# Kernel tuning notes

Hardware: AMD Instinct MI355X
Metric: run time of the kernel (lower is better)

The kernel has to match this reference:

```python
import jax, jax.numpy as jnp
import numpy as np

B, T, C = 2, 2048, 1024
NUM_HEADS, NUM_KV_HEADS, HEAD_DIM = 16, 8, 64
R = NUM_HEADS // NUM_KV_HEADS  # q heads per kv head
WINDOW = 512
HIDDEN = 4096
SOFT_CAP = 50.0


def setup_inputs() -> dict:
    key = jax.random.key(0)
    ks = jax.random.split(key, 10)
    std = 0.02
    return {
        "x": jax.random.normal(ks[0], (B, T, C), jnp.float32),
        "kurtosis_sum": jnp.zeros((), jnp.float32),
        "rms1_scale": jnp.zeros((C,), jnp.float32),
        "q_kernel": std * jax.random.normal(ks[1], (C, R, NUM_KV_HEADS, HEAD_DIM), jnp.float32),
        "k_kernel": std * jax.random.normal(ks[2], (C, NUM_KV_HEADS, HEAD_DIM), jnp.float32),
        "v_kernel": std * jax.random.normal(ks[3], (C, NUM_KV_HEADS, HEAD_DIM), jnp.float32),
        "out_kernel": std * jax.random.normal(ks[4], (R, NUM_KV_HEADS, HEAD_DIM, C), jnp.float32),
        "rms2_scale": jnp.zeros((C,), jnp.float32),
        "gate_kernel": std * jax.random.normal(ks[5], (C, HIDDEN), jnp.float32),
        "up_kernel": std * jax.random.normal(ks[6], (C, HIDDEN), jnp.float32),
        "down_kernel": std * jax.random.normal(ks[7], (HIDDEN, C), jnp.float32),
    }


def sine_table(features, length, max_timescale=1e6):
    fraction = jnp.arange(0, features, 2, dtype=jnp.float32) / features
    rot_freq = 1.0 / (max_timescale ** fraction)
    sinusoid = jnp.arange(length, dtype=jnp.float32)[:, None] * rot_freq[None, :]
    sinusoid = jnp.concatenate([sinusoid, sinusoid], axis=-1)  # (T, features)
    return jnp.sin(sinusoid), jnp.cos(sinusoid)


def rotate_half(x):
    x1, x2 = jnp.split(x, 2, axis=-1)
    return jnp.concatenate([-x2, x1], axis=-1)


def rms_norm(x, scale):
    var = jnp.mean(jnp.square(x.astype(jnp.float32)), axis=-1, keepdims=True)
    normed = (x * jax.lax.rsqrt(var + 1e-6)).astype(x.dtype)
    return normed * (1 + scale)


def excess_kurtosis(emb):
    mean = jnp.mean(emb, axis=-1, keepdims=True)
    std = jnp.std(emb, axis=-1, keepdims=True)
    centralized = emb - mean
    fourth = jnp.mean(centralized ** 4, axis=-1, keepdims=True)
    kurt = jnp.squeeze(fourth / (std ** 4 + 1e-6), axis=-1).reshape(-1) - 3
    return jnp.sum(jnp.maximum(kurt, 0.0))


def reference(x, kurtosis_sum, rms1_scale, q_kernel, k_kernel, v_kernel,
              out_kernel, rms2_scale, gate_kernel, up_kernel, down_kernel):
    Bc, Tc, Cc = x.shape
    # sliding-window causal mask: j <= i and |i - j| < WINDOW
    idx = jnp.arange(Tc)
    causal = idx[:, None] >= idx[None, :]
    band = jnp.abs(idx[:, None] - idx[None, :]) < WINDOW
    mask = (causal & band)[None, None, None]  # (1,1,1,T,T) for brhsd scores

    # --- attention ---
    attn_in = rms_norm(x, rms1_scale)
    q = jnp.einsum('bsm,mrhk->brhsk', attn_in, q_kernel)
    k = jnp.einsum('bdm,mhk->bhdk', attn_in, k_kernel)
    v = jnp.einsum('bdm,mhv->bhdv', attn_in, v_kernel)

    sin, cos = sine_table(HEAD_DIM, Tc, max_timescale=1e6)
    q = q * cos[None, None, None] + rotate_half(q) * sin[None, None, None]
    k = k * cos[None, None] + rotate_half(k) * sin[None, None]

    scale = jax.lax.rsqrt(jnp.asarray(HEAD_DIM, dtype=x.dtype))
    qk = jnp.einsum('brhsk,bhdk->brhsd', q, k) * scale
    qk = jnp.tanh(qk / SOFT_CAP) * SOFT_CAP
    probs = jax.nn.softmax(qk.astype(jnp.float32), where=mask).astype(x.dtype)
    qkv = jnp.einsum('brhsd,bhdv->brhsv', probs, v)
    attn_out = jnp.einsum('brhsv,rhvm->bsm', qkv, out_kernel)
    x = x + attn_out

    # --- SwiGLU MLP ---
    mlp_in = rms_norm(x, rms2_scale)
    gate = jax.nn.silu(mlp_in @ gate_kernel)
    up = mlp_in @ up_kernel
    x = x + (up * gate) @ down_kernel

    return (x, kurtosis_sum + excess_kurtosis(x))
```

## Files before the change

### kernel.cpp

```cpp
#include <hip/hip_runtime.h>
#include <hip/hip_bf16.h>

typedef __attribute__((ext_vector_type(8))) short short8;
typedef __attribute__((ext_vector_type(4))) float f32x4;
typedef __attribute__((ext_vector_type(4))) int int4v;
typedef __attribute__((ext_vector_type(8))) int int8v;

#define DEVFN static __device__ __forceinline__

DEVFN float bf2f(unsigned short u) {
    unsigned int i = ((unsigned int)u) << 16;
    float f; __builtin_memcpy(&f, &i, 4); return f;
}
DEVFN unsigned short f2bf(float f) {
    unsigned int i; __builtin_memcpy(&i, &f, 4);
    unsigned int r = i + 0x7fffu + ((i >> 16) & 1u);
    return (unsigned short)(r >> 16);
}
DEVFN unsigned char f2fp8(float f) {
    int r = __builtin_amdgcn_cvt_pk_fp8_f32(f, f, 0, false);
    return (unsigned char)(r & 0xff);
}
DEVFN float fastrcp(float x) { return __builtin_amdgcn_rcpf(x); }

DEVFN void load_lds16(const void* g, void* l) {
    __builtin_amdgcn_global_load_lds(
        (__attribute__((address_space(1))) void*)g,
        (__attribute__((address_space(3))) void*)l, 16, 0, 0);
}

DEVFN f32x4 mfma_fp8(int8v a, int8v b, f32x4 c) {
    return __builtin_amdgcn_mfma_scale_f32_16x16x128_f8f6f4(
        a, b, c, 0, 0, 0, 0x7F7F7F7F, 0, 0x7F7F7F7F);
}

constexpr int Bsz = 2, T = 2048, C = 1024;
constexpr int NH = 16, NKV = 8, HD = 64;
constexpr int HID = 4096;
constexpr int NTOK = Bsz * T;
constexpr size_t MiB = 1024 * 1024;

constexpr size_t OFF_WQKV = 0;
constexpr size_t OFF_WOUT = 4 * MiB;
constexpr size_t OFF_WGATE = 6 * MiB;
constexpr size_t OFF_WUP = 10 * MiB;
constexpr size_t OFF_WDOWN = 14 * MiB;
constexpr size_t OFF_XN1 = 18 * MiB;
constexpr size_t OFF_QKVP = 26 * MiB;
constexpr size_t OFF_P2 = 26 * MiB;
constexpr size_t OFF_QB = 58 * MiB;
constexpr size_t OFF_KB = 66 * MiB;
constexpr size_t OFF_VT = 70 * MiB;
constexpr size_t OFF_CTX = 74 * MiB;
constexpr size_t OFF_X2 = 82 * MiB;
constexpr size_t OFF_XN2 = 98 * MiB;
constexpr size_t OFF_G = 102 * MiB;
constexpr size_t OFF_P4 = 118 * MiB;

__global__ __launch_bounds__(256) void prep_kernel(
    const float* __restrict__ qk, const float* __restrict__ kk2,
    const float* __restrict__ vk, const float* __restrict__ ok,
    const float* __restrict__ gk, const float* __restrict__ uk,
    const float* __restrict__ dk,
    unsigned short* __restrict__ wqkv, unsigned short* __restrict__ wout,
    unsigned char* __restrict__ wgate, unsigned char* __restrict__ wup,
    unsigned char* __restrict__ wdown,
    const float* __restrict__ x, const float* __restrict__ rms1_scale,
    unsigned short* __restrict__ xn1) {
    __shared__ float t[32][33];
    __shared__ float red[4];
    int id = blockIdx.x;
    int tid = threadIdx.x;
    if (id >= 15360) {
        int row = id - 15360;
        const float4 v = *(const float4*)&x[(size_t)row * 1024 + tid * 4];
        float ss = v.x * v.x + v.y * v.y + v.z * v.z + v.w * v.w;
#pragma unroll
        for (int m = 32; m; m >>= 1) ss += __shfl_xor(ss, m, 64);
        if ((tid & 63) == 0) red[tid >> 6] = ss;
        __syncthreads();
        float tot = red[0] + red[1] + red[2] + red[3];
        float inv = rsqrtf(tot * (1.f / 1024.f) + 1e-6f);
        const float4 sc = *(const float4*)&rms1_scale[tid * 4];
        size_t o = (size_t)row * 1024 + tid * 4;
        xn1[o + 0] = f2bf(v.x * inv * (1.f + sc.x));
        xn1[o + 1] = f2bf(v.y * inv * (1.f + sc.y));
        xn1[o + 2] = f2bf(v.z * inv * (1.f + sc.z));
        xn1[o + 3] = f2bf(v.w * inv * (1.f + sc.w));
        return;
    }
    const float* in; int K, N, nx, base; int fp8 = 0;
    unsigned short* out16 = nullptr; unsigned char* out8 = nullptr;
    if (id < 1024)       { in = qk;  out16 = wqkv;                       K = 1024; N = 1024; nx = 32;  base = 0; }
    else if (id < 1536)  { in = kk2; out16 = wqkv + (size_t)1024 * 1024; K = 1024; N = 512;  nx = 16;  base = 1024; }
    else if (id < 2048)  { in = vk;  out16 = wqkv + (size_t)1536 * 1024; K = 1024; N = 512;  nx = 16;  base = 1536; }
    else if (id < 3072)  { in = ok;  out16 = wout;                       K = 1024; N = 1024; nx = 32;  base = 2048; }
    else if (id < 7168)  { in = gk;  out8 = wgate; fp8 = 1;              K = 1024; N = 4096; nx = 128; base = 3072; }
    else if (id < 11264) { in = uk;  out8 = wup; fp8 = 1;                K = 1024; N = 4096; nx = 128; base = 7168; }
    else                 { in = dk;  out8 = wdown; fp8 = 1;              K = 4096; N = 1024; nx = 32;  base = 11264; }
    int lid = id - base;
    int n0 = (lid % nx) * 32, k0 = (lid / nx) * 32;
    int tx = tid & 31, ty = tid >> 5;
#pragma unroll
    for (int i = 0; i < 4; i++)
        t[ty + 8 * i][tx] = in[(size_t)(k0 + ty + 8 * i) * N + n0 + tx];
    __syncthreads();
    if (fp8) {
#pragma unroll
        for (int i = 0; i < 4; i++)
            out8[(size_t)(n0 + ty + 8 * i) * K + k0 + tx] = f2fp8(t[tx][ty + 8 * i] * 16.f);
    } else {
#pragma unroll
        for (int i = 0; i < 4; i++)
            out16[(size_t)(n0 + ty + 8 * i) * K + k0 + tx] = f2bf(t[tx][ty + 8 * i]);
    }
}

__global__ __launch_bounds__(256) void gemm128(const unsigned short* __restrict__ A,
                                               const unsigned short* __restrict__ Bt,
                                               unsigned short* __restrict__ Cp,
                                               int N, int K, int lda, int ldb,
                                               size_t zA, size_t zB, size_t zC) {
    __shared__ __align__(16) unsigned short As[128 * 32];
    __shared__ __align__(16) unsigned short Bs[128 * 32];
    A += (size_t)blockIdx.z * zA;
    Bt += (size_t)blockIdx.z * zB;
    const int tid = threadIdx.x;
    const int lane = tid & 63, w = tid >> 6;
    const int quad = lane >> 4, l15 = lane & 15;
    const int wr = w >> 1, wc = w & 1;
    const int m0 = blockIdx.y * 128, n0 = blockIdx.x * 128;

    f32x4 acc[4][4];
#pragma unroll
    for (int i = 0; i < 4; i++)
#pragma unroll
        for (int j = 0; j < 4; j++) acc[i][j] = f32x4{0.f, 0.f, 0.f, 0.f};

    const int stRow = (w << 4) + (lane >> 2);
    const int stCol = (lane & 3) << 3;

    for (int kk = 0; kk < K; kk += 32) {
#pragma unroll
        for (int i = 0; i < 2; i++) {
            load_lds16(A + (size_t)(m0 + (i << 6) + stRow) * lda + kk + stCol,
                       &As[((i << 6) + (w << 4)) * 32]);
            load_lds16(Bt + (size_t)(n0 + (i << 6) + stRow) * ldb + kk + stCol,
                       &Bs[((i << 6) + (w << 4)) * 32]);
        }
        __syncthreads();
        short8 a[4], b[4];
#pragma unroll
        for (int mi = 0; mi < 4; mi++)
            a[mi] = *(const short8*)&As[(wr * 64 + mi * 16 + l15) * 32 + quad * 8];
#pragma unroll
        for (int ni = 0; ni < 4; ni++)
            b[ni] = *(const short8*)&Bs[(wc * 64 + ni * 16 + l15) * 32 + quad * 8];
#pragma unroll
        for (int mi = 0; mi < 4; mi++)
#pragma unroll
            for (int ni = 0; ni < 4; ni++)
                acc[mi][ni] = __builtin_amdgcn_mfma_f32_16x16x32_bf16(a[mi], b[ni], acc[mi][ni], 0, 0, 0);
        __syncthreads();
    }
#pragma unroll
    for (int mi = 0; mi < 4; mi++)
#pragma unroll
        for (int ni = 0; ni < 4; ni++)
#pragma unroll
            for (int r = 0; r < 4; r++) {
                int row = m0 + wr * 64 + mi * 16 + quad * 4 + r;
                int col = n0 + wc * 64 + ni * 16 + l15;
                Cp[(size_t)blockIdx.z * zC + (size_t)row * N + col] = f2bf(acc[mi][ni][r]);
            }
}

DEVFN int8v read_frag8(const unsigned char* buf, int rb, int quad) {
    int base = rb * 128;
    int h0 = (2 * quad) ^ (rb & 7);
    int h1 = (2 * quad + 1) ^ (rb & 7);
    int4v lo = *(const int4v*)&buf[base + h0 * 16];
    int4v hi = *(const int4v*)&buf[base + h1 * 16];
    return int8v{lo.x, lo.y, lo.z, lo.w, hi.x, hi.y, hi.z, hi.w};
}

__global__ __launch_bounds__(256) void gateup_kernel(const unsigned char* __restrict__ A,
                                                     const unsigned char* __restrict__ Bg,
                                                     const unsigned char* __restrict__ Bu,
                                                     unsigned char* __restrict__ out) {
    __shared__ __align__(16) unsigned char As[2][128 * 128];
    __shared__ __align__(16) unsigned char Gs[2][64 * 128];
    __shared__ __align__(16) unsigned char Us[2][64 * 128];
    const int tid = threadIdx.x;
    const int lane = tid & 63, w = tid >> 6;
    const int quad = lane >> 4, l15 = lane & 15;
    const int wr = w >> 1, wc = w & 1;
    const int m0 = blockIdx.y * 128, n0 = blockIdx.x * 64;

    f32x4 aG[4][2], aU[4][2];
#pragma unroll
    for (int i = 0; i < 4; i++)
#pragma unroll
        for (int j = 0; j < 2; j++) { aG[i][j] = f32x4{0.f, 0.f, 0.f, 0.f}; aU[i][j] = f32x4{0.f, 0.f, 0.f, 0.f}; }

    const int lrow = lane >> 3;
    const int hA = (lane & 7) ^ lrow;

    auto STAGE = [&](int t, int b) {
#pragma unroll
        for (int j = 0; j < 4; j++) {
            int i = w * 4 + j;
            int r = i * 8 + lrow;
            load_lds16(A + (size_t)(m0 + r) * 1024 + t * 128 + hA * 16, &As[b][i * 1024]);
        }
#pragma unroll
        for (int j = 0; j < 2; j++) {
            int i = w * 2 + j;
            int r = i * 8 + lrow;
            load_lds16(Bg + (size_t)(n0 + r) * 1024 + t * 128 + hA * 16, &Gs[b][i * 1024]);
            load_lds16(Bu + (size_t)(n0 + r) * 1024 + t * 128 + hA * 16, &Us[b][i * 1024]);
        }
    };

    STAGE(0, 0);
    STAGE(1, 1);

#pragma unroll
    for (int t = 0; t < 8; ++t) {
        if (t < 7) asm volatile("s_waitcnt vmcnt(8)\n\ts_barrier" ::: "memory");
        else       asm volatile("s_waitcnt vmcnt(0)\n\ts_barrier" ::: "memory");
        const int b = t & 1;
        int8v a[4], bg[2], bu[2];
#pragma unroll
        for (int mi = 0; mi < 4; mi++)
            a[mi] = read_frag8(As[b], wr * 64 + mi * 16 + l15, quad);
#pragma unroll
        for (int ni = 0; ni < 2; ni++) {
            bg[ni] = read_frag8(Gs[b], wc * 32 + ni * 16 + l15, quad);
            bu[ni] = read_frag8(Us[b], wc * 32 + ni * 16 + l15, quad);
        }
        asm volatile("s_waitcnt lgkmcnt(0)\n\ts_barrier" ::: "memory");
        if (t < 6) STAGE(t + 2, b);
        __builtin_amdgcn_sched_barrier(0);
        __builtin_amdgcn_s_setprio(1);
#pragma unroll
        for (int mi = 0; mi < 4; mi++)
#pragma unroll
            for (int ni = 0; ni < 2; ni++) {
                aG[mi][ni] = mfma_fp8(a[mi], bg[ni], aG[mi][ni]);
                aU[mi][ni] = mfma_fp8(a[mi], bu[ni], aU[mi][ni]);
            }
        __builtin_amdgcn_s_setprio(0);
    }
#pragma unroll
    for (int mi = 0; mi < 4; mi++)
#pragma unroll
        for (int ni = 0; ni < 2; ni++)
#pragma unroll
            for (int r = 0; r < 4; r++) {
                int row = m0 + wr * 64 + mi * 16 + quad * 4 + r;
                int col = n0 + wc * 32 + ni * 16 + l15;
                float vg = aG[mi][ni][r] * (1.f / 64.f);
                float vu = aU[mi][ni][r] * (1.f / 64.f);
                float s = vg * fastrcp(1.f + __expf(-vg));
                out[(size_t)row * 4096 + col] = f2fp8(s * vu * 8.f);
            }
}

__global__ __launch_bounds__(256) void down_gemm(const unsigned char* __restrict__ A,
                                                 const unsigned char* __restrict__ Bt,
                                                 unsigned short* __restrict__ Cp) {
    __shared__ __align__(16) unsigned char As[2][128 * 128];
    __shared__ __align__(16) unsigned char Bs[2][128 * 128];
    const int tid = threadIdx.x;
    const int lane = tid & 63, w = tid >> 6;
    const int quad = lane >> 4, l15 = lane & 15;
    const int wr = w >> 1, wc = w & 1;
    const int m0 = blockIdx.y * 128, n0 = blockIdx.x * 128;
    const int kbase = blockIdx.z * 2048;

    f32x4 acc[4][4];
#pragma unroll
    for (int i = 0; i < 4; i++)
#pragma unroll
        for (int j = 0; j < 4; j++) acc[i][j] = f32x4{0.f, 0.f, 0.f, 0.f};

    const int lrow = lane >> 3;
    const int hA = (lane & 7) ^ lrow;

    auto STAGE = [&](int t, int b) {
#pragma unroll
        for (int j = 0; j < 4; j++) {
            int i = w * 4 + j;
            int r = i * 8 + lrow;
            load_lds16(A + (size_t)(m0 + r) * 4096 + kbase + t * 128 + hA * 16, &As[b][i * 1024]);
            load_lds16(Bt + (size_t)(n0 + r) * 4096 + kbase + t * 128 + hA * 16, &Bs[b][i * 1024]);
        }
    };

    STAGE(0, 0);
    STAGE(1, 1);

#pragma unroll
    for (int t = 0; t < 16; ++t) {
        if (t < 15) asm volatile("s_waitcnt vmcnt(8)\n\ts_barrier" ::: "memory");
        else        asm volatile("s_waitcnt vmcnt(0)\n\ts_barrier" ::: "memory");
        const int b = t & 1;
        int8v a[4], bb[4];
#pragma unroll
        for (int mi = 0; mi < 4; mi++)
            a[mi] = read_frag8(As[b], wr * 64 + mi * 16 + l15, quad);
#pragma unroll
        for (int ni = 0; ni < 4; ni++)
            bb[ni] = read_frag8(Bs[b], wc * 64 + ni * 16 + l15, quad);
        asm volatile("s_waitcnt lgkmcnt(0)\n\ts_barrier" ::: "memory");
        if (t < 14) STAGE(t + 2, b);
        __builtin_amdgcn_sched_barrier(0);
        __builtin_amdgcn_s_setprio(1);
#pragma unroll
        for (int mi = 0; mi < 4; mi++)
#pragma unroll
            for (int ni = 0; ni < 4; ni++)
                acc[mi][ni] = mfma_fp8(a[mi], bb[ni], acc[mi][ni]);
        __builtin_amdgcn_s_setprio(0);
    }
    const size_t Z = (size_t)NTOK * 1024;
#pragma unroll
    for (int mi = 0; mi < 4; mi++)
#pragma unroll
        for (int ni = 0; ni < 4; ni++)
#pragma unroll
            for (int r = 0; r < 4; r++) {
                int row = m0 + wr * 64 + mi * 16 + quad * 4 + r;
                int col = n0 + wc * 64 + ni * 16 + l15;
                Cp[(size_t)blockIdx.z * Z + (size_t)row * 1024 + col] =
                    f2bf(acc[mi][ni][r] * (1.f / 128.f));
            }
}

__global__ __launch_bounds__(256) void reduce_out(const unsigned short* __restrict__ p,
                                                  const float* __restrict__ x,
                                                  const float* __restrict__ scale,
                                                  float* __restrict__ x2,
                                                  unsigned char* __restrict__ xn2,
                                                  const float* __restrict__ ksum,
                                                  float* __restrict__ outk) {
    __shared__ float red[4];
    int row = blockIdx.x, tid = threadIdx.x;
    if (row == 0 && tid == 0) outk[0] = ksum[0];
    size_t base = (size_t)row * 1024 + tid * 4;
    const size_t Z = (size_t)NTOK * 1024;
    float4 v = *(const float4*)&x[base];
#pragma unroll
    for (int z = 0; z < 2; z++) {
        ushort4 u = *(const ushort4*)&p[base + z * Z];
        v.x += bf2f(u.x); v.y += bf2f(u.y); v.z += bf2f(u.z); v.w += bf2f(u.w);
    }
    *(float4*)&x2[base] = v;
    float ss = v.x * v.x + v.y * v.y + v.z * v.z + v.w * v.w;
#pragma unroll
    for (int m = 32; m; m >>= 1) ss += __shfl_xor(ss, m, 64);
    if ((tid & 63) == 0) red[tid >> 6] = ss;
    __syncthreads();
    float tot = red[0] + red[1] + red[2] + red[3];
    float inv = rsqrtf(tot * (1.f / 1024.f) + 1e-6f) * 4.f;
    const float4 sc = *(const float4*)&scale[tid * 4];
    xn2[base + 0] = f2fp8(v.x * inv * (1.f + sc.x));
    xn2[base + 1] = f2fp8(v.y * inv * (1.f + sc.y));
    xn2[base + 2] = f2fp8(v.z * inv * (1.f + sc.z));
    xn2[base + 3] = f2fp8(v.w * inv * (1.f + sc.w));
}

__global__ __launch_bounds__(256) void reduce_down(const unsigned short* __restrict__ p,
                                                   const float* __restrict__ x2,
                                                   float* __restrict__ outx,
                                                   float* __restrict__ outk) {
    __shared__ float red[4], r2[4], r4[4];
    int row = blockIdx.x, tid = threadIdx.x;
    size_t base = (size_t)row * 1024 + tid * 4;
    const size_t Z = (size_t)NTOK * 1024;
    float4 v = *(const float4*)&x2[base];
#pragma unroll
    for (int z = 0; z < 2; z++) {
        ushort4 u = *(const ushort4*)&p[base + z * Z];
        v.x += bf2f(u.x); v.y += bf2f(u.y); v.z += bf2f(u.z); v.w += bf2f(u.w);
    }
    *(float4*)&outx[base] = v;
    float s = v.x + v.y + v.z + v.w;
#pragma unroll
    for (int m = 32; m; m >>= 1) s += __shfl_xor(s, m, 64);
    if ((tid & 63) == 0) red[tid >> 6] = s;
    __syncthreads();
    float mean = (red[0] + red[1] + red[2] + red[3]) * (1.f / 1024.f);
    float cx = v.x - mean, cy = v.y - mean, cz = v.z - mean, cw = v.w - mean;
    float x2v = cx * cx, y2 = cy * cy, z2 = cz * cz, w2 = cw * cw;
    float c2 = x2v + y2 + z2 + w2;
    float c4 = x2v * x2v + y2 * y2 + z2 * z2 + w2 * w2;
#pragma unroll
    for (int m = 32; m; m >>= 1) {
        c2 += __shfl_xor(c2, m, 64);
        c4 += __shfl_xor(c4, m, 64);
    }
    if ((tid & 63) == 0) { r2[tid >> 6] = c2; r4[tid >> 6] = c4; }
    __syncthreads();
    if (tid == 0) {
        float m2 = (r2[0] + r2[1] + r2[2] + r2[3]) * (1.f / 1024.f);
        float m4 = (r4[0] + r4[1] + r4[2] + r4[3]) * (1.f / 1024.f);
        float kurt = m4 / (m2 * m2 + 1e-6f) - 3.f;
        if (kurt > 0.f) atomicAdd(outk, kurt);
    }
}

__global__ __launch_bounds__(256) void ropevt_kernel(const unsigned short* __restrict__ qkvp,
                                                     unsigned short* __restrict__ qb,
                                                     unsigned short* __restrict__ kb,
                                                     unsigned short* __restrict__ vt) {
    __shared__ float sv[32], cv[32];
    __shared__ unsigned short tile[64][68];
    int id = blockIdx.x;
    int tid = threadIdx.x;
    if (id < NTOK) {
        int tok = id;
        int b = tok >> 11, t = tok & 2047;
        if (tid < 32) {
            float fr = (float)tid * (1.f / 32.f);
            float freq = powf(1e6f, -fr);
            float a = (float)t * freq;
            sv[tid] = sinf(a);
            cv[tid] = cosf(a);
        }
        __syncthreads();
        const unsigned short* r0 = qkvp + (size_t)tok * 2048;
#pragma unroll
        for (int e = tid; e < 1536; e += 256) {
            int u = e >> 6, d = e & 63;
            int col = (u < 16) ? (u * 64 + d) : (1024 + (u - 16) * 64 + d);
            int pcol = (d < 32) ? col + 32 : col - 32;
            float sgn = (d < 32) ? -1.f : 1.f;
            float vc = bf2f(r0[col]);
            float vp = bf2f(r0[pcol]);
            float o = vc * cv[d & 31] + sgn * vp * sv[d & 31];
            if (u < 16)
                qb[((size_t)(b * 16 + u) * 2048 + t) * 64 + d] = f2bf(o);
            else
                kb[((size_t)(b * 8 + (u - 16)) * 2048 + t) * 64 + d] = f2bf(o);
        }
    } else {
        int lid = id - NTOK;
        int b = lid >> 8, h = (lid >> 5) & 7, t0 = (lid & 31) * 64;
        int d = tid & 63, tr = tid >> 6;
#pragma unroll
        for (int i = 0; i < 16; i++) {
            int t = tr + i * 4;
            size_t gi = (size_t)(b * 2048 + t0 + t) * 2048 + 1536 + h * 64 + d;
            tile[t][d] = qkvp[gi];
        }
        __syncthreads();
        int tt = tid & 63, dr = tid >> 6;
#pragma unroll
        for (int i = 0; i < 16; i++) {
            int dd = dr + i * 4;
            vt[((size_t)(b * 8 + h) * 64 + dd) * 2048 + t0 + tt] = tile[tt][dd];
        }
    }
}

__global__ __launch_bounds__(256) void attn_kernel(const unsigned short* __restrict__ qb,
                                                   const unsigned short* __restrict__ kb,
                                                   const unsigned short* __restrict__ vt,
                                                   unsigned short* __restrict__ ctx) {
    __shared__ __align__(16) unsigned short Ks[64 * 64];
    __shared__ __align__(16) unsigned short Vs[64 * 64];
    __shared__ __align__(16) unsigned short P[4][2][16 * 64];
    const int tid = threadIdx.x, lane = tid & 63, w = tid >> 6;
    const int quad = lane >> 4, l15 = lane & 15;
    const int qt = blockIdx.x, H = blockIdx.y, b = blockIdx.z;
    const int hkv = H & 7;
    const int qw = qt * 64 + w * 16;

    const unsigned short* qbase = qb + ((size_t)(b * 16 + H) * 2048 + qw) * 64;
    short8 aq0 = *(const short8*)(qbase + (size_t)l15 * 64 + quad * 8);
    short8 aq1 = *(const short8*)(qbase + (size_t)l15 * 64 + 32 + quad * 8);

    const unsigned short* kbase = kb + (size_t)(b * 8 + hkv) * 2048 * 64;
    const unsigned short* vbase = vt + (size_t)(b * 8 + hkv) * 64 * 2048;

    const short bf1 = (short)0x3F80;
    const short8 ones = {bf1, bf1, bf1, bf1, bf1, bf1, bf1, bf1};

    f32x4 O[4];
#pragma unroll
    for (int i = 0; i < 4; i++) O[i] = f32x4{0.f, 0.f, 0.f, 0.f};
    f32x4 lacc = f32x4{0.f, 0.f, 0.f, 0.f};

    const int srow = lane >> 3;
    const int schunk = (lane & 7) ^ srow;
    const int sw = l15 & 7;

    int kstartB = qt * 64 - 511;
    if (kstartB < 0) kstartB = 0;
    kstartB &= ~63;
    const int kendB = qt * 64 + 63;
    int buf = 0;

    for (int k0 = kstartB; k0 <= kendB; k0 += 64) {
#pragma unroll
        for (int rr = 0; rr < 2; rr++) {
            int row = w * 8 + rr * 32 + srow;
            load_lds16(kbase + (size_t)(k0 + row) * 64 + schunk * 8,
                       &Ks[(w * 8 + rr * 32) * 64]);
            load_lds16(vbase + (size_t)row * 2048 + k0 + schunk * 8,
                       &Vs[(w * 8 + rr * 32) * 64]);
        }
        __syncthreads();
        f32x4 S[4];
#pragma unroll
        for (int c = 0; c < 4; c++) {
            const unsigned short* kp = &Ks[(c * 16 + l15) * 64];
            short8 kf0 = *(const short8*)&kp[(quad ^ sw) * 8];
            short8 kf1 = *(const short8*)&kp[((4 + quad) ^ sw) * 8];
            f32x4 s = __builtin_amdgcn_mfma_f32_16x16x32_bf16(aq0, kf0, f32x4{0.f, 0.f, 0.f, 0.f}, 0, 0, 0);
            s = __builtin_amdgcn_mfma_f32_16x16x32_bf16(aq1, kf1, s, 0, 0, 0);
            S[c] = s;
        }
        unsigned short* Pw = P[w][buf];
#pragma unroll
        for (int c = 0; c < 4; c++)
#pragma unroll
            for (int r = 0; r < 4; r++) {
                int i = qw + quad * 4 + r;
                int j = k0 + c * 16 + l15;
                float Sc = fminf(3200.f, fmaxf(-3200.f, S[c][r]));
                float e = __expf(Sc * 0.005f);
                float y = 50.f - 100.f * fastrcp(e + 1.f);
                bool ok = (j <= i) && ((i - j) < 512);
                float pv = ok ? __expf(y) : 0.f;
                Pw[(quad * 4 + r) * 64 + c * 16 + l15] = f2bf(pv);
            }
        asm volatile("s_waitcnt lgkmcnt(0)" ::: "memory");
        short8 pf0 = *(const short8*)&Pw[l15 * 64 + quad * 8];
        short8 pf1 = *(const short8*)&Pw[l15 * 64 + 32 + quad * 8];
#pragma unroll
        for (int ni = 0; ni < 4; ni++) {
            const unsigned short* vp = &Vs[(ni * 16 + l15) * 64];
            short8 vf0 = *(const short8*)&vp[(quad ^ sw) * 8];
            short8 vf1 = *(const short8*)&vp[((4 + quad) ^ sw) * 8];
            O[ni] = __builtin_amdgcn_mfma_f32_16x16x32_bf16(pf0, vf0, O[ni], 0, 0, 0);
            O[ni] = __builtin_amdgcn_mfma_f32_16x16x32_bf16(pf1, vf1, O[ni], 0, 0, 0);
        }
        lacc = __builtin_amdgcn_mfma_f32_16x16x32_bf16(pf0, ones, lacc, 0, 0, 0);
        lacc = __builtin_amdgcn_mfma_f32_16x16x32_bf16(pf1, ones, lacc, 0, 0, 0);
        buf ^= 1;
        __syncthreads();
    }
#pragma unroll
    for (int r = 0; r < 4; r++) {
        float inv = fastrcp(lacc[r]);
        int i = qw + quad * 4 + r;
        size_t tok = (size_t)b * 2048 + i;
#pragma unroll
        for (int ni = 0; ni < 4; ni++)
            ctx[tok * 1024 + H * 64 + ni * 16 + l15] = f2bf(O[ni][r] * inv);
    }
}

extern "C" void kernel_launch(void* const* d_in, const int* in_sizes, int n_in,
                              void* d_out, int out_size, void* d_ws, size_t ws_size,
                              hipStream_t stream) {
    const float* x = (const float*)d_in[0];
    const float* ksum = (const float*)d_in[1];
    const float* rms1_scale = (const float*)d_in[2];
    const float* q_w = (const float*)d_in[3];
    const float* k_w = (const float*)d_in[4];
    const float* v_w = (const float*)d_in[5];
    const float* out_w = (const float*)d_in[6];
    const float* rms2_scale = (const float*)d_in[7];
    const float* gate_w = (const float*)d_in[8];
    const float* up_w = (const float*)d_in[9];
    const float* down_w = (const float*)d_in[10];

    char* ws = (char*)d_ws;
    unsigned short* wqkv = (unsigned short*)(ws + OFF_WQKV);
    unsigned short* wout = (unsigned short*)(ws + OFF_WOUT);
    unsigned char* wgate = (unsigned char*)(ws + OFF_WGATE);
    unsigned char* wup = (unsigned char*)(ws + OFF_WUP);
    unsigned char* wdown = (unsigned char*)(ws + OFF_WDOWN);
    unsigned short* xn1 = (unsigned short*)(ws + OFF_XN1);
    unsigned short* qkvp = (unsigned short*)(ws + OFF_QKVP);
    unsigned short* p2 = (unsigned short*)(ws + OFF_P2);
    unsigned short* qb = (unsigned short*)(ws + OFF_QB);
    unsigned short* kb = (unsigned short*)(ws + OFF_KB);
    unsigned short* vtb = (unsigned short*)(ws + OFF_VT);
    unsigned short* ctx = (unsigned short*)(ws + OFF_CTX);
    float* x2 = (float*)(ws + OFF_X2);
    unsigned char* xn2 = (unsigned char*)(ws + OFF_XN2);
    unsigned char* g = (unsigned char*)(ws + OFF_G);
    unsigned short* p4 = (unsigned short*)(ws + OFF_P4);
    float* outx = (float*)d_out;
    float* outk = outx + (size_t)NTOK * C;

    prep_kernel<<<15360 + NTOK, 256, 0, stream>>>(
        q_w, k_w, v_w, out_w, gate_w, up_w, down_w,
        wqkv, wout, wgate, wup, wdown, x, rms1_scale, xn1);

    gemm128<<<dim3(2048 / 128, NTOK / 128, 1), 256, 0, stream>>>(
        xn1, wqkv, qkvp, 2048, 1024, 1024, 1024, 0, 0, 0);

    ropevt_kernel<<<NTOK + 512, 256, 0, stream>>>(qkvp, qb, kb, vtb);

    attn_kernel<<<dim3(T / 64, NH, Bsz), 256, 0, stream>>>(qb, kb, vtb, ctx);

    gemm128<<<dim3(1024 / 128, NTOK / 128, 2), 256, 0, stream>>>(
        ctx, wout, p2, 1024, 512, 1024, 1024, 512, 512, (size_t)NTOK * 1024);
    reduce_out<<<NTOK, 256, 0, stream>>>(p2, x, rms2_scale, x2, xn2, ksum, outk);

    gateup_kernel<<<dim3(HID / 64, NTOK / 128), 256, 0, stream>>>(xn2, wgate, wup, g);

    down_gemm<<<dim3(1024 / 128, NTOK / 128, 2), 256, 0, stream>>>(g, wdown, p4);
    reduce_down<<<NTOK, 256, 0, stream>>>(p4, x2, outx, outk);

    (void)in_sizes; (void)n_in; (void)out_size; (void)ws_size;
}
```

Baseline: 324.5 us.

## Fuse RoPE into QKV GEMM epilogue and double-buffer bf16 GEMM LDS

The QKV projection gets its own GEMM kernel that applies RoPE in the epilogue and writes Q and K directly in head-major layout, with the sin/cos table precomputed once in the prep kernel. V is written to a compact buffer and transposed by a separate smaller kernel. This removes the full round trip of the intermediate QKV buffer through global memory. Both bf16 GEMMs also gain double-buffered LDS staging with explicit waitcnt and barriers plus raised priority around the MFMA block, overlapping global loads with compute at the cost of twice the shared memory.

```diff
diff --git a/kernel.cpp b/kernel.cpp
--- a/kernel.cpp
+++ b/kernel.cpp
@@ -46,7 +46,7 @@
 constexpr size_t OFF_WUP = 10 * MiB;
 constexpr size_t OFF_WDOWN = 14 * MiB;
 constexpr size_t OFF_XN1 = 18 * MiB;
-constexpr size_t OFF_QKVP = 26 * MiB;
+constexpr size_t OFF_VBUF = 26 * MiB;
 constexpr size_t OFF_P2 = 26 * MiB;
 constexpr size_t OFF_QB = 58 * MiB;
 constexpr size_t OFF_KB = 66 * MiB;
@@ -56,6 +56,8 @@
 constexpr size_t OFF_XN2 = 98 * MiB;
 constexpr size_t OFF_G = 102 * MiB;
 constexpr size_t OFF_P4 = 118 * MiB;
+constexpr size_t OFF_ST = 134 * MiB;
+constexpr size_t OFF_CT = 134 * MiB + 256 * 1024;
 
 __global__ __launch_bounds__(256) void prep_kernel(
     const float* __restrict__ qk, const float* __restrict__ kk2,
@@ -66,11 +68,21 @@
     unsigned char* __restrict__ wgate, unsigned char* __restrict__ wup,
     unsigned char* __restrict__ wdown,
     const float* __restrict__ x, const float* __restrict__ rms1_scale,
-    unsigned short* __restrict__ xn1) {
+    unsigned short* __restrict__ xn1,
+    float* __restrict__ st, float* __restrict__ ct) {
     __shared__ float t[32][33];
     __shared__ float red[4];
     int id = blockIdx.x;
     int tid = threadIdx.x;
+    if (id >= 19456) {
+        int idx = (id - 19456) * 256 + tid;
+        float fr = (float)(idx & 31) * (1.f / 32.f);
+        float freq = powf(1e6f, -fr);
+        float a = (float)(idx >> 5) * freq;
+        st[idx] = sinf(a);
+        ct[idx] = cosf(a);
+        return;
+    }
     if (id >= 15360) {
         int row = id - 15360;
         const float4 v = *(const float4*)&x[(size_t)row * 1024 + tid * 4];
@@ -121,8 +133,8 @@
                                                unsigned short* __restrict__ Cp,
                                                int N, int K, int lda, int ldb,
                                                size_t zA, size_t zB, size_t zC) {
-    __shared__ __align__(16) unsigned short As[128 * 32];
-    __shared__ __align__(16) unsigned short Bs[128 * 32];
+    __shared__ __align__(16) unsigned short As[2][128 * 32];
+    __shared__ __align__(16) unsigned short Bs[2][128 * 32];
     A += (size_t)blockIdx.z * zA;
     Bt += (size_t)blockIdx.z * zB;
     const int tid = threadIdx.x;
@@ -140,28 +152,40 @@
     const int stRow = (w << 4) + (lane >> 2);
     const int stCol = (lane & 3) << 3;
 
-    for (int kk = 0; kk < K; kk += 32) {
+    auto STAGE = [&](int kk, int b) {
 #pragma unroll
         for (int i = 0; i < 2; i++) {
             load_lds16(A + (size_t)(m0 + (i << 6) + stRow) * lda + kk + stCol,
-                       &As[((i << 6) + (w << 4)) * 32]);
+                       &As[b][((i << 6) + (w << 4)) * 32]);
             load_lds16(Bt + (size_t)(n0 + (i << 6) + stRow) * ldb + kk + stCol,
-                       &Bs[((i << 6) + (w << 4)) * 32]);
-        }
-        __syncthreads();
-        short8 a[4], b[4];
-#pragma unroll
-        for (int mi = 0; mi < 4; mi++)
-            a[mi] = *(const short8*)&As[(wr * 64 + mi * 16 + l15) * 32 + quad * 8];
+                       &Bs[b][((i << 6) + (w << 4)) * 32]);
+        }
+    };
+
+    const int nsteps = K >> 5;
+    STAGE(0, 0);
+    STAGE(32, 1);
+    for (int s = 0; s < nsteps; ++s) {
+        if (s < nsteps - 1) asm volatile("s_waitcnt vmcnt(4)\n\ts_barrier" ::: "memory");
+        else                asm volatile("s_waitcnt vmcnt(0)\n\ts_barrier" ::: "memory");
+        const int b = s & 1;
+        short8 a[4], bf[4];
+#pragma unroll
+        for (int mi = 0; mi < 4; mi++)
+            a[mi] = *(const short8*)&As[b][(wr * 64 + mi * 16 + l15) * 32 + quad * 8];
 #pragma unroll
         for (int ni = 0; ni < 4; ni++)
-            b[ni] = *(const short8*)&Bs[(wc * 64 + ni * 16 + l15) * 32 + quad * 8];
+            bf[ni] = *(const short8*)&Bs[b][(wc * 64 + ni * 16 + l15) * 32 + quad * 8];
+        asm volatile("s_waitcnt lgkmcnt(0)\n\ts_barrier" ::: "memory");
+        if (s + 2 < nsteps) STAGE((s + 2) * 32, b);
+        __builtin_amdgcn_sched_barrier(0);
+        __builtin_amdgcn_s_setprio(1);
 #pragma unroll
         for (int mi = 0; mi < 4; mi++)
 #pragma unroll
             for (int ni = 0; ni < 4; ni++)
-                acc[mi][ni] = __builtin_amdgcn_mfma_f32_16x16x32_bf16(a[mi], b[ni], acc[mi][ni], 0, 0, 0);
-        __syncthreads();
+                acc[mi][ni] = __builtin_amdgcn_mfma_f32_16x16x32_bf16(a[mi], bf[ni], acc[mi][ni], 0, 0, 0);
+        __builtin_amdgcn_s_setprio(0);
     }
 #pragma unroll
     for (int mi = 0; mi < 4; mi++)
@@ -173,6 +197,122 @@
                 int col = n0 + wc * 64 + ni * 16 + l15;
                 Cp[(size_t)blockIdx.z * zC + (size_t)row * N + col] = f2bf(acc[mi][ni][r]);
             }
+}
+
+__global__ __launch_bounds__(256) void gemm_qkv(const unsigned short* __restrict__ A,
+                                                const unsigned short* __restrict__ Bt,
+                                                unsigned short* __restrict__ qb,
+                                                unsigned short* __restrict__ kb,
+                                                unsigned short* __restrict__ vbuf,
+                                                const float* __restrict__ st,
+                                                const float* __restrict__ ct) {
+    __shared__ __align__(16) unsigned short As[2][128 * 32];
+    __shared__ __align__(16) unsigned short Bs[2][128 * 32];
+    const int tid = threadIdx.x;
+    const int lane = tid & 63, w = tid >> 6;
+    const int quad = lane >> 4, l15 = lane & 15;
+    const int wr = w >> 1, wc = w & 1;
+    const int m0 = blockIdx.y * 128, n0 = blockIdx.x * 128;
+
+    f32x4 acc[4][4];
+#pragma unroll
+    for (int i = 0; i < 4; i++)
+#pragma unroll
+        for (int j = 0; j < 4; j++) acc[i][j] = f32x4{0.f, 0.f, 0.f, 0.f};
+
+    const int stRow = (w << 4) + (lane >> 2);
+    const int stCol = (lane & 3) << 3;
+
+    auto STAGE = [&](int kk, int b) {
+#pragma unroll
+        for (int i = 0; i < 2; i++) {
+            load_lds16(A + (size_t)(m0 + (i << 6) + stRow) * 1024 + kk + stCol,
+                       &As[b][((i << 6) + (w << 4)) * 32]);
+            load_lds16(Bt + (size_t)(n0 + (i << 6) + stRow) * 1024 + kk + stCol,
+                       &Bs[b][((i << 6) + (w << 4)) * 32]);
+        }
+    };
+
+    STAGE(0, 0);
+    STAGE(32, 1);
+    for (int s = 0; s < 32; ++s) {
+        if (s < 31) asm volatile("s_waitcnt vmcnt(4)\n\ts_barrier" ::: "memory");
+        else        asm volatile("s_waitcnt vmcnt(0)\n\ts_barrier" ::: "memory");
+        const int b = s & 1;
+        short8 a[4], bf[4];
+#pragma unroll
+        for (int mi = 0; mi < 4; mi++)
+            a[mi] = *(const short8*)&As[b][(wr * 64 + mi * 16 + l15) * 32 + quad * 8];
+#pragma unroll
+        for (int ni = 0; ni < 4; ni++)
+            bf[ni] = *(const short8*)&Bs[b][(wc * 64 + ni * 16 + l15) * 32 + quad * 8];
+        asm volatile("s_waitcnt lgkmcnt(0)\n\ts_barrier" ::: "memory");
+        if (s < 30) STAGE((s + 2) * 32, b);
+        __builtin_amdgcn_sched_barrier(0);
+        __builtin_amdgcn_s_setprio(1);
+#pragma unroll
+        for (int mi = 0; mi < 4; mi++)
+#pragma unroll
+            for (int ni = 0; ni < 4; ni++)
+                acc[mi][ni] = __builtin_amdgcn_mfma_f32_16x16x32_bf16(a[mi], bf[ni], acc[mi][ni], 0, 0, 0);
+        __builtin_amdgcn_s_setprio(0);
+    }
+
+    if (n0 < 1536) {
+        const int head = (n0 + wc * 64) >> 6;
+        const bool isq = head < 16;
+        unsigned short* ob = isq ? qb : kb;
+        const int hb = isq ? head : head - 16;
+        const int hn = isq ? 16 : 8;
+#pragma unroll
+        for (int ni = 0; ni < 2; ni++) {
+            const int d = ni * 16 + l15;
+#pragma unroll
+            for (int mi = 0; mi < 4; mi++)
+#pragma unroll
+                for (int r = 0; r < 4; r++) {
+                    int row = m0 + wr * 64 + mi * 16 + quad * 4 + r;
+                    int t = row & 2047, bb = row >> 11;
+                    float c = ct[t * 32 + d], sv = st[t * 32 + d];
+                    float x1 = acc[mi][ni][r], x2 = acc[mi][ni + 2][r];
+                    size_t obase = ((size_t)(bb * hn + hb) * 2048 + t) * 64;
+                    ob[obase + d]      = f2bf(x1 * c - x2 * sv);
+                    ob[obase + d + 32] = f2bf(x2 * c + x1 * sv);
+                }
+        }
+    } else {
+#pragma unroll
+        for (int mi = 0; mi < 4; mi++)
+#pragma unroll
+            for (int ni = 0; ni < 4; ni++)
+#pragma unroll
+                for (int r = 0; r < 4; r++) {
+                    int row = m0 + wr * 64 + mi * 16 + quad * 4 + r;
+                    int col = n0 - 1536 + wc * 64 + ni * 16 + l15;
+                    vbuf[(size_t)row * 512 + col] = f2bf(acc[mi][ni][r]);
+                }
+    }
+}
+
+__global__ __launch_bounds__(256) void vtrans_kernel(const unsigned short* __restrict__ vbuf,
+                                                     unsigned short* __restrict__ vt) {
+    __shared__ unsigned short tile[64][68];
+    int lid = blockIdx.x;
+    int tid = threadIdx.x;
+    int b = lid >> 8, h = (lid >> 5) & 7, t0 = (lid & 31) * 64;
+    int d = tid & 63, tr = tid >> 6;
+#pragma unroll
+    for (int i = 0; i < 16; i++) {
+        int t = tr + i * 4;
+        tile[t][d] = vbuf[(size_t)(b * 2048 + t0 + t) * 512 + h * 64 + d];
+    }
+    __syncthreads();
+    int tt = tid & 63, dr = tid >> 6;
+#pragma unroll
+    for (int i = 0; i < 16; i++) {
+        int dd = dr + i * 4;
+        vt[((size_t)(b * 8 + h) * 64 + dd) * 2048 + t0 + tt] = tile[tt][dd];
+    }
 }
 
 DEVFN int8v read_frag8(const unsigned char* buf, int rb, int quad) {
@@ -408,60 +548,6 @@
         float m4 = (r4[0] + r4[1] + r4[2] + r4[3]) * (1.f / 1024.f);
         float kurt = m4 / (m2 * m2 + 1e-6f) - 3.f;
         if (kurt > 0.f) atomicAdd(outk, kurt);
-    }
-}
-
-__global__ __launch_bounds__(256) void ropevt_kernel(const unsigned short* __restrict__ qkvp,
-                                                     unsigned short* __restrict__ qb,
-                                                     unsigned short* __restrict__ kb,
-                                                     unsigned short* __restrict__ vt) {
-    __shared__ float sv[32], cv[32];
-    __shared__ unsigned short tile[64][68];
-    int id = blockIdx.x;
-    int tid = threadIdx.x;
-    if (id < NTOK) {
-        int tok = id;
-        int b = tok >> 11, t = tok & 2047;
-        if (tid < 32) {
-            float fr = (float)tid * (1.f / 32.f);
-            float freq = powf(1e6f, -fr);
-            float a = (float)t * freq;
-            sv[tid] = sinf(a);
-            cv[tid] = cosf(a);
-        }
-        __syncthreads();
-        const unsigned short* r0 = qkvp + (size_t)tok * 2048;
-#pragma unroll
-        for (int e = tid; e < 1536; e += 256) {
-            int u = e >> 6, d = e & 63;
-            int col = (u < 16) ? (u * 64 + d) : (1024 + (u - 16) * 64 + d);
-            int pcol = (d < 32) ? col + 32 : col - 32;
-            float sgn = (d < 32) ? -1.f : 1.f;
-            float vc = bf2f(r0[col]);
-            float vp = bf2f(r0[pcol]);
-            float o = vc * cv[d & 31] + sgn * vp * sv[d & 31];
-            if (u < 16)
-                qb[((size_t)(b * 16 + u) * 2048 + t) * 64 + d] = f2bf(o);
-            else
-                kb[((size_t)(b * 8 + (u - 16)) * 2048 + t) * 64 + d] = f2bf(o);
-        }
-    } else {
-        int lid = id - NTOK;
-        int b = lid >> 8, h = (lid >> 5) & 7, t0 = (lid & 31) * 64;
-        int d = tid & 63, tr = tid >> 6;
-#pragma unroll
-        for (int i = 0; i < 16; i++) {
-            int t = tr + i * 4;
-            size_t gi = (size_t)(b * 2048 + t0 + t) * 2048 + 1536 + h * 64 + d;
-            tile[t][d] = qkvp[gi];
-        }
-        __syncthreads();
-        int tt = tid & 63, dr = tid >> 6;
-#pragma unroll
-        for (int i = 0; i < 16; i++) {
-            int dd = dr + i * 4;
-            vt[((size_t)(b * 8 + h) * 64 + dd) * 2048 + t0 + tt] = tile[tt][dd];
-        }
     }
 }
 
@@ -586,7 +672,7 @@
     unsigned char* wup = (unsigned char*)(ws + OFF_WUP);
     unsigned char* wdown = (unsigned char*)(ws + OFF_WDOWN);
     unsigned short* xn1 = (unsigned short*)(ws + OFF_XN1);
-    unsigned short* qkvp = (unsigned short*)(ws + OFF_QKVP);
+    unsigned short* vbuf = (unsigned short*)(ws + OFF_VBUF);
     unsigned short* p2 = (unsigned short*)(ws + OFF_P2);
     unsigned short* qb = (unsigned short*)(ws + OFF_QB);
     unsigned short* kb = (unsigned short*)(ws + OFF_KB);
@@ -596,17 +682,19 @@
     unsigned char* xn2 = (unsigned char*)(ws + OFF_XN2);
     unsigned char* g = (unsigned char*)(ws + OFF_G);
     unsigned short* p4 = (unsigned short*)(ws + OFF_P4);
+    float* st = (float*)(ws + OFF_ST);
+    float* ct = (float*)(ws + OFF_CT);
     float* outx = (float*)d_out;
     float* outk = outx + (size_t)NTOK * C;
 
-    prep_kernel<<<15360 + NTOK, 256, 0, stream>>>(
+    prep_kernel<<<19712, 256, 0, stream>>>(
         q_w, k_w, v_w, out_w, gate_w, up_w, down_w,
-        wqkv, wout, wgate, wup, wdown, x, rms1_scale, xn1);
-
-    gemm128<<<dim3(2048 / 128, NTOK / 128, 1), 256, 0, stream>>>(
-        xn1, wqkv, qkvp, 2048, 1024, 1024, 1024, 0, 0, 0);
-
-    ropevt_kernel<<<NTOK + 512, 256, 0, stream>>>(qkvp, qb, kb, vtb);
+        wqkv, wout, wgate, wup, wdown, x, rms1_scale, xn1, st, ct);
+
+    gemm_qkv<<<dim3(2048 / 128, NTOK / 128), 256, 0, stream>>>(
+        xn1, wqkv, qb, kb, vbuf, st, ct);
+
+    vtrans_kernel<<<512, 256, 0, stream>>>(vbuf, vtb);
 
     attn_kernel<<<dim3(T / 64, NH, Bsz), 256, 0, stream>>>(qb, kb, vtb, ctx);
 
```

Result: faster. 314.2 us (-3.2%).
